# Kernel optimization log

Measured on AMD Instinct MI355X. Metric: run time of the kernel, lower is better.

The kernel has to match this reference:

```python
import jax, jax.numpy as jnp
import numpy as np

HIDDEN = 4096
N_HEADS = 32
N_KV_HEADS = 8
HEAD_DIM = HIDDEN // N_HEADS  # 128
N_GROUPS = N_HEADS // N_KV_HEADS  # 4
ROPE_THETA = 10000.0
BSZ, SEQ = 2, 2048


def rotate_half(x):
    x1 = x[..., : x.shape[-1] // 2]
    x2 = x[..., x.shape[-1] // 2 :]
    return jnp.concatenate((-x2, x1), axis=-1)


def rope_tables(seq_len, head_dim, theta):
    inv_freq = 1.0 / theta ** (jnp.arange(0, head_dim, 2, dtype=jnp.float32) / head_dim)
    t = jnp.arange(seq_len, dtype=jnp.float32)
    freqs = jnp.einsum('i,j->ij', t, inv_freq)          # [S, head_dim/2]
    emb = jnp.concatenate((freqs, freqs), axis=-1)       # [S, head_dim]
    return jnp.cos(emb), jnp.sin(emb)


def setup_inputs() -> dict:
    key = jax.random.key(0)
    ks = jax.random.split(key, 5)
    hidden_states = jax.random.normal(ks[0], (BSZ, SEQ, HIDDEN), dtype=jnp.float32)
    # causal additive mask [B, 1, Q, K]
    causal = jnp.tril(jnp.ones((SEQ, SEQ), dtype=bool))
    attention_mask = jnp.where(causal, 0.0, -1e9).astype(jnp.float32)
    attention_mask = jnp.broadcast_to(attention_mask[None, None], (BSZ, 1, SEQ, SEQ))
    position_ids = jnp.broadcast_to(jnp.arange(SEQ, dtype=jnp.int32)[None, :], (BSZ, SEQ))
    sc = 1.0 / np.sqrt(HIDDEN)
    Wq = jax.random.normal(ks[1], (HIDDEN, N_HEADS * HEAD_DIM), dtype=jnp.float32) * sc
    Wk = jax.random.normal(ks[2], (HIDDEN, N_KV_HEADS * HEAD_DIM), dtype=jnp.float32) * sc
    Wv = jax.random.normal(ks[3], (HIDDEN, N_KV_HEADS * HEAD_DIM), dtype=jnp.float32) * sc
    Wo = jax.random.normal(ks[4], (N_HEADS * HEAD_DIM, HIDDEN), dtype=jnp.float32) * sc
    return {
        'hidden_states': hidden_states,
        'attention_mask': attention_mask,
        'position_ids': position_ids,
        'Wq': Wq, 'Wk': Wk, 'Wv': Wv, 'Wo': Wo,
    }


def reference(hidden_states, attention_mask, position_ids, Wq, Wk, Wv, Wo):
    bsz, q_len, _ = hidden_states.shape
    # QKV projections
    q = (hidden_states @ Wq).reshape(bsz, q_len, N_HEADS, HEAD_DIM).swapaxes(1, 2)       # [B,H,S,D]
    k = (hidden_states @ Wk).reshape(bsz, q_len, N_KV_HEADS, HEAD_DIM).swapaxes(1, 2)    # [B,Hkv,S,D]
    v = (hidden_states @ Wv).reshape(bsz, q_len, N_KV_HEADS, HEAD_DIM).swapaxes(1, 2)    # [B,Hkv,S,D]
    # RoPE
    cos_t, sin_t = rope_tables(q_len, HEAD_DIM, ROPE_THETA)
    cos = jnp.take(cos_t, position_ids, axis=0)[:, None]  # [B,1,S,D]
    sin = jnp.take(sin_t, position_ids, axis=0)[:, None]
    q = q * cos + rotate_half(q) * sin
    k = k * cos + rotate_half(k) * sin
    # GQA attention via grouped einsum (equivalent to repeat_kv, without materializing repeats)
    qg = q.reshape(bsz, N_KV_HEADS, N_GROUPS, q_len, HEAD_DIM)
    scores = jnp.einsum('bhgqd,bhkd->bhgqk', qg, k) / jnp.sqrt(jnp.float32(HEAD_DIM))
    scores = scores + attention_mask[:, :, None]  # broadcast mask over (kv_head, group)
    probs = jax.nn.softmax(scores.astype(jnp.float32), axis=-1).astype(hidden_states.dtype)
    out = jnp.einsum('bhgqk,bhkd->bhgqd', probs, v)
    out = out.reshape(bsz, N_HEADS, q_len, HEAD_DIM).swapaxes(1, 2).reshape(bsz, q_len, HIDDEN)
    return out @ Wo
```

## Files before the change

### kernel.cpp

```cpp
#include <hip/hip_runtime.h>
#include <hip/hip_bf16.h>
#include <cstdint>

#define HIDDEN 4096
#define NH 32
#define NKV 8
#define HD 128
#define SEQ 2048
#define BSZ 2
#define QKVN 6144
#define QKVLD 6144

using bf16x8 = __attribute__((ext_vector_type(8))) short;
using f32x4  = __attribute__((ext_vector_type(4))) float;
using f32x16 = __attribute__((ext_vector_type(16))) float;

__device__ __forceinline__ ushort f2bf(float f) {
  union { float f; uint32_t u; } v; v.f = f;
  uint32_t r = (v.u + 0x7FFFu + ((v.u >> 16) & 1u)) >> 16;
  return (ushort)r;
}
__device__ __forceinline__ float bf2f(ushort s) {
  union { uint32_t u; float f; } v; v.u = ((uint32_t)s) << 16;
  return v.f;
}

__device__ __forceinline__ uint32_t cvtpk(float lo, float hi) {
  uint32_t r;
  asm("v_cvt_pk_bf16_f32 %0, %1, %2" : "=v"(r) : "v"(lo), "v"(hi));
  return r;
}
__device__ __forceinline__ void pl32swap(uint32_t& a, uint32_t& b) {
  asm("v_permlane32_swap_b32 %0, %1" : "+v"(a), "+v"(b));
}

__device__ __forceinline__ void gload_lds16(const void* g, void* l) {
  __builtin_amdgcn_global_load_lds(
      (const __attribute__((address_space(1))) void*)g,
      (__attribute__((address_space(3))) void*)l, 16, 0, 0);
}

__global__ __launch_bounds__(256)
void cvt_bf16_kernel(const float* __restrict__ X, ushort* __restrict__ Xb, int n8) {
  int t = blockIdx.x * 256 + threadIdx.x;
  if (t >= n8) return;
  size_t i = (size_t)t * 8;
  float4 a = *(const float4*)(X + i);
  float4 b = *(const float4*)(X + i + 4);
  uint4 p;
  p.x = (uint)f2bf(a.x) | ((uint)f2bf(a.y) << 16);
  p.y = (uint)f2bf(a.z) | ((uint)f2bf(a.w) << 16);
  p.z = (uint)f2bf(b.x) | ((uint)f2bf(b.y) << 16);
  p.w = (uint)f2bf(b.z) | ((uint)f2bf(b.w) << 16);
  *(uint4*)(Xb + i) = p;
}

__global__ __launch_bounds__(256)
void transpose_bf16_kernel(const float* __restrict__ W, ushort* __restrict__ WT,
                           int K, int N) {
  __shared__ ushort tile[64][72];
  const int k0 = blockIdx.y * 64, n0 = blockIdx.x * 64;
  const int tr = threadIdx.x >> 4;
  const int tc = (threadIdx.x & 15) * 4;
#pragma unroll
  for (int i = 0; i < 4; ++i) {
    const int k = tr + i * 16;
    float4 v = *(const float4*)(W + (size_t)(k0 + k) * N + n0 + tc);
    ushort4 u;
    u.x = f2bf(v.x); u.y = f2bf(v.y); u.z = f2bf(v.z); u.w = f2bf(v.w);
    *(ushort4*)&tile[k][tc] = u;
  }
  __syncthreads();
  const int nr = threadIdx.x >> 3;
  const int kc = (threadIdx.x & 7) * 8;
#pragma unroll
  for (int i = 0; i < 2; ++i) {
    const int n = nr + i * 32;
    bf16x8 o;
#pragma unroll
    for (int j = 0; j < 8; ++j) o[j] = tile[kc + j][n];
    *(bf16x8*)(WT + (size_t)(n0 + n) * K + k0 + kc) = o;
  }
}

__global__ __launch_bounds__(256)
void transpose_v_kernel(const ushort* __restrict__ Vsrc, ushort* __restrict__ VtG) {
  __shared__ ushort tile[64][72];
  const int slice = blockIdx.z;
  const int b = slice >> 3, kh = slice & 7;
  const int s0 = blockIdx.x * 64, d0 = blockIdx.y * 64;
  const ushort* src = Vsrc + ((size_t)(b * SEQ) + s0) * QKVLD + kh * HD + d0;
  const int sr = threadIdx.x >> 3;
  const int dc = (threadIdx.x & 7) * 8;
#pragma unroll
  for (int i = 0; i < 2; ++i) {
    const int s = sr + i * 32;
    *(bf16x8*)&tile[s][dc] = *(const bf16x8*)(src + (size_t)s * QKVLD + dc);
  }
  __syncthreads();
  ushort* dst = VtG + ((size_t)slice * HD + d0) * SEQ + s0;
  const int dr = threadIdx.x >> 3;
  const int sc = (threadIdx.x & 7) * 8;
#pragma unroll
  for (int i = 0; i < 2; ++i) {
    const int d = dr + i * 32;
    bf16x8 o;
#pragma unroll
    for (int j = 0; j < 8; ++j) o[j] = tile[sc + j][d];
    *(bf16x8*)(dst + (size_t)d * SEQ + sc) = o;
  }
}

__global__ __launch_bounds__(512, 2)
void gemmqkv_kernel(const ushort* __restrict__ A, const ushort* __restrict__ BT,
                    ushort* __restrict__ Cp, int M, int N, int K) {
  extern __shared__ ushort lds[];
  const int tid = threadIdx.x, lane = tid & 63, wave = tid >> 6;
  const int l15 = lane & 15, l4 = lane >> 4;
  const int wr = wave >> 2, wc = wave & 3;

  const int mt = M >> 8, ntile = N / 192, nwg = mt * ntile;
  const int swq = nwg >> 3, swr = nwg & 7;
  const int xcd = blockIdx.x & 7, lo = blockIdx.x >> 3;
  const int wg = (xcd < swr ? xcd * (swq + 1) : swr * (swq + 1) + (xcd - swr) * swq) + lo;
  const int m0 = (wg % mt) << 8;
  const int n0 = (wg / mt) * 192;

  ushort* LA[2][2];
  ushort* LB[2][2];
#pragma unroll
  for (int b_ = 0; b_ < 2; ++b_)
#pragma unroll
    for (int s_ = 0; s_ < 2; ++s_) {
      LA[b_][s_] = lds + (b_ * 2 + s_) * 8192;
      LB[b_][s_] = lds + 32768 + (b_ * 2 + s_) * 6144;
    }

  const ushort* Abase = A + (size_t)m0 * K;
  const ushort* Bbase = BT + (size_t)n0 * K;

  const int srow0 = tid >> 2;
  const int scol8 = (((tid & 3) ^ ((srow0 >> 1) & 3)) << 3);
  const int bs1 = tid;
  const int brow1 = bs1 >> 2;
  const int bcol1 = (((bs1 & 3) ^ ((bs1 >> 3) & 3)) << 3);
  const int bs2 = 512 + wave * 32 + (lane & 31);
  const int brow2 = bs2 >> 2;
  const int bcol2 = (((bs2 & 3) ^ ((bs2 >> 3) & 3)) << 3);

  const int swb  = (l4 ^ ((l15 >> 1) & 3)) << 3;
  const int aoff = (wr * 128 + l15) * 32 + swb;
  const int boff = (wc * 48 + l15) * 32 + swb;

  f32x4 acc[8][3] = {};
  bf16x8 a[4];
  bf16x8 b[3];

#define STAGE_EV(buf, ks, kt)                                                  \
  do {                                                                         \
    const size_t gc_ = (size_t)(kt) * 64 + (ks) * 32;                          \
    gload_lds16(Abase + (size_t)srow0 * K + gc_ + scol8,                       \
                &LA[buf][ks][tid * 8]);                                        \
    gload_lds16(Bbase + (size_t)brow1 * K + gc_ + bcol1,                       \
                &LB[buf][ks][tid * 8]);                                        \
  } while (0)

#define STAGE_OD(buf, ks, kt)                                                  \
  do {                                                                         \
    const size_t gc_ = (size_t)(kt) * 64 + (ks) * 32;                          \
    gload_lds16(Abase + (size_t)(128 + srow0) * K + gc_ + scol8,               \
                &LA[buf][ks][(512 + tid) * 8]);                                \
    if ((lane & 32) == 0)                                                      \
      gload_lds16(Bbase + (size_t)brow2 * K + gc_ + bcol2,                     \
                  &LB[buf][ks][(512 + wave * 32 + (lane & 31)) * 8]);          \
  } while (0)

#define MFMA_ __builtin_amdgcn_mfma_f32_16x16x32_bf16

#define PHASE_EVEN(buf, ks, sb, sk, skt)                                       \
  {                                                                            \
    _Pragma("unroll") for (int m_ = 0; m_ < 4; ++m_)                           \
      a[m_] = *(const bf16x8*)&LA[buf][ks][aoff + m_ * 512];                   \
    _Pragma("unroll") for (int n_ = 0; n_ < 3; ++n_)                           \
      b[n_] = *(const bf16x8*)&LB[buf][ks][boff + n_ * 512];                   \
    STAGE_EV(sb, sk, skt);                                                     \
    asm volatile("s_barrier" ::: "memory");                                    \
    __builtin_amdgcn_s_setprio(1);                                             \
    _Pragma("unroll") for (int m_ = 0; m_ < 4; ++m_)                           \
      _Pragma("unroll") for (int n_ = 0; n_ < 3; ++n_)                         \
        acc[m_][n_] = MFMA_(a[m_], b[n_], acc[m_][n_], 0, 0, 0);               \
    __builtin_amdgcn_s_setprio(0);                                             \
    asm volatile("s_barrier" ::: "memory");                                    \
  }

#define PHASE_ODD(buf, ks, sb, sk, skt)                                        \
  {                                                                            \
    _Pragma("unroll") for (int m_ = 0; m_ < 4; ++m_)                           \
      a[m_] = *(const bf16x8*)&LA[buf][ks][aoff + (4 + m_) * 512];             \
    STAGE_OD(sb, sk, skt);                                                     \
    asm volatile("s_barrier" ::: "memory");                                    \
    __builtin_amdgcn_s_setprio(1);                                             \
    _Pragma("unroll") for (int m_ = 0; m_ < 4; ++m_)                           \
      _Pragma("unroll") for (int n_ = 0; n_ < 3; ++n_)                         \
        acc[4 + m_][n_] = MFMA_(a[m_], b[n_], acc[4 + m_][n_], 0, 0, 0);       \
    __builtin_amdgcn_s_setprio(0);                                             \
    asm volatile("s_waitcnt vmcnt(8)");                                        \
    asm volatile("s_barrier" ::: "memory");                                    \
  }

  const int NT = K >> 6;

  STAGE_EV(0, 0, 0); STAGE_OD(0, 0, 0);
  STAGE_EV(0, 1, 0); STAGE_OD(0, 1, 0);
  STAGE_EV(1, 0, 1); STAGE_OD(1, 0, 1);
  asm volatile("s_waitcnt vmcnt(8)");
  asm volatile("s_barrier" ::: "memory");

  for (int i = 0; i < (NT >> 1); ++i) {
    const int kt0 = 2 * i;
    const int ktA = (kt0 + 2 < NT) ? kt0 + 2 : NT - 1;
    const int ktB = (kt0 + 3 < NT) ? kt0 + 3 : NT - 1;
    PHASE_EVEN(0, 0, 1, 1, kt0 + 1)
    PHASE_ODD (0, 0, 1, 1, kt0 + 1)
    PHASE_EVEN(0, 1, 0, 0, ktA)
    PHASE_ODD (0, 1, 0, 0, ktA)
    PHASE_EVEN(1, 0, 0, 1, ktA)
    PHASE_ODD (1, 0, 0, 1, ktA)
    PHASE_EVEN(1, 1, 1, 0, ktB)
    PHASE_ODD (1, 1, 1, 0, ktB)
  }
#undef PHASE_EVEN
#undef PHASE_ODD
#undef STAGE_EV
#undef STAGE_OD

  const int crow0 = m0 + wr * 128 + l4 * 4;
  const int ccol0 = n0 + wc * 48 + l15;
#pragma unroll
  for (int m_ = 0; m_ < 8; ++m_)
#pragma unroll
    for (int n_ = 0; n_ < 3; ++n_)
#pragma unroll
      for (int r_ = 0; r_ < 4; ++r_) {
        const size_t row = crow0 + m_ * 16 + r_;
        const int col = ccol0 + n_ * 16;
        Cp[row * N + col] = f2bf(acc[m_][n_][r_]);
      }
}

template<int OUT_BF16>
__global__ __launch_bounds__(512, 2)
void gemm8p_kernel(const ushort* __restrict__ A, const ushort* __restrict__ BT,
                   void* __restrict__ Cp, int M, int N, int K) {
  extern __shared__ ushort lds[];
  const int tid = threadIdx.x, lane = tid & 63, wave = tid >> 6;
  const int l15 = lane & 15, l4 = lane >> 4;
  const int wr = wave >> 2, wc = wave & 3;

  const int mt = M >> 8, nt = N >> 8, nwg = mt * nt;
  const int swq = nwg >> 3, swr = nwg & 7;
  const int xcd = blockIdx.x & 7, lo = blockIdx.x >> 3;
  const int wg = (xcd < swr ? xcd * (swq + 1) : swr * (swq + 1) + (xcd - swr) * swq) + lo;
  const int m0 = (wg % mt) << 8;
  const int n0 = (wg / mt) << 8;

  ushort* LA[2][2];
  ushort* LB[2][2];
#pragma unroll
  for (int b_ = 0; b_ < 2; ++b_)
#pragma unroll
    for (int s_ = 0; s_ < 2; ++s_) {
      LA[b_][s_] = lds + ((b_ * 2 + 0) * 2 + s_) * 8192;
      LB[b_][s_] = lds + ((b_ * 2 + 1) * 2 + s_) * 8192;
    }

  const ushort* Abase = A + (size_t)m0 * K;
  const ushort* Bbase = BT + (size_t)n0 * K;

  const int srow0 = tid >> 2;
  const int scol8 = (((tid & 3) ^ ((srow0 >> 1) & 3)) << 3);

  const int swb  = (l4 ^ ((l15 >> 1) & 3)) << 3;
  const int aoff = (wr * 128 + l15) * 32 + swb;
  const int boff = (wc * 64 + l15) * 32 + swb;

  f32x4 acc[8][4] = {};
  bf16x8 a[4];
  bf16x8 b[4];

#define STAGE(buf, ks, kt, part)                                              \
  do {                                                                        \
    const size_t gc_ = (size_t)(kt) * 64 + (ks) * 32 + scol8;                 \
    const int rw_ = srow0 + (part) * 128;                                     \
    const int dst_ = ((part) * 512 + tid) * 8;                                \
    gload_lds16(Abase + (size_t)rw_ * K + gc_, &LA[buf][ks][dst_]);           \
    gload_lds16(Bbase + (size_t)rw_ * K + gc_, &LB[buf][ks][dst_]);           \
  } while (0)

#define MFMA_ __builtin_amdgcn_mfma_f32_16x16x32_bf16

#define PHASE_EVEN(buf, ks, sb, sk, skt)                                      \
  {                                                                           \
    _Pragma("unroll") for (int m_ = 0; m_ < 4; ++m_)                          \
      a[m_] = *(const bf16x8*)&LA[buf][ks][aoff + m_ * 512];                  \
    _Pragma("unroll") for (int n_ = 0; n_ < 4; ++n_)                          \
      b[n_] = *(const bf16x8*)&LB[buf][ks][boff + n_ * 512];                  \
    STAGE(sb, sk, skt, 0);                                                    \
    asm volatile("s_barrier" ::: "memory");                                   \
    __builtin_amdgcn_s_setprio(1);                                            \
    _Pragma("unroll") for (int m_ = 0; m_ < 4; ++m_)                          \
      _Pragma("unroll") for (int n_ = 0; n_ < 4; ++n_)                        \
        acc[m_][n_] = MFMA_(a[m_], b[n_], acc[m_][n_], 0, 0, 0);              \
    __builtin_amdgcn_s_setprio(0);                                            \
    asm volatile("s_barrier" ::: "memory");                                   \
  }

#define PHASE_ODD(buf, ks, sb, sk, skt)                                       \
  {                                                                           \
    _Pragma("unroll") for (int m_ = 0; m_ < 4; ++m_)                          \
      a[m_] = *(const bf16x8*)&LA[buf][ks][aoff + (4 + m_) * 512];            \
    STAGE(sb, sk, skt, 1);                                                    \
    asm volatile("s_barrier" ::: "memory");                                   \
    __builtin_amdgcn_s_setprio(1);                                            \
    _Pragma("unroll") for (int m_ = 0; m_ < 4; ++m_)                          \
      _Pragma("unroll") for (int n_ = 0; n_ < 4; ++n_)                        \
        acc[4 + m_][n_] = MFMA_(a[m_], b[n_], acc[4 + m_][n_], 0, 0, 0);      \
    __builtin_amdgcn_s_setprio(0);                                            \
    asm volatile("s_waitcnt vmcnt(8)");                                       \
    asm volatile("s_barrier" ::: "memory");                                   \
  }

  const int NT = K >> 6;

  STAGE(0, 0, 0, 0); STAGE(0, 0, 0, 1);
  STAGE(0, 1, 0, 0); STAGE(0, 1, 0, 1);
  STAGE(1, 0, 1, 0); STAGE(1, 0, 1, 1);
  asm volatile("s_waitcnt vmcnt(8)");
  asm volatile("s_barrier" ::: "memory");

  for (int i = 0; i < (NT >> 1); ++i) {
    const int kt0 = 2 * i;
    const int ktA = (kt0 + 2 < NT) ? kt0 + 2 : NT - 1;
    const int ktB = (kt0 + 3 < NT) ? kt0 + 3 : NT - 1;
    PHASE_EVEN(0, 0, 1, 1, kt0 + 1)
    PHASE_ODD (0, 0, 1, 1, kt0 + 1)
    PHASE_EVEN(0, 1, 0, 0, ktA)
    PHASE_ODD (0, 1, 0, 0, ktA)
    PHASE_EVEN(1, 0, 0, 1, ktA)
    PHASE_ODD (1, 0, 0, 1, ktA)
    PHASE_EVEN(1, 1, 1, 0, ktB)
    PHASE_ODD (1, 1, 1, 0, ktB)
  }
#undef PHASE_EVEN
#undef PHASE_ODD
#undef STAGE

  const int crow0 = m0 + wr * 128 + l4 * 4;
  const int ccol0 = n0 + wc * 64 + l15;
#pragma unroll
  for (int m_ = 0; m_ < 8; ++m_)
#pragma unroll
    for (int n_ = 0; n_ < 4; ++n_)
#pragma unroll
      for (int r_ = 0; r_ < 4; ++r_) {
        const size_t row = crow0 + m_ * 16 + r_;
        const int col = ccol0 + n_ * 16;
        const float val = acc[m_][n_][r_];
        if (OUT_BF16) ((ushort*)Cp)[row * N + col] = f2bf(val);
        else          ((float*)Cp)[row * N + col]  = val;
      }
}

__global__ __launch_bounds__(256)
void rope_qk_kernel(ushort* qkv, const int* __restrict__ pos_ids, int total) {
  int t = blockIdx.x * 256 + threadIdx.x;
  if (t >= total) return;
  int j = t & 63;
  int rest = t >> 6;
  int hp = rest % 40;
  int bs = rest / 40;
  float pos = (float)pos_ids[bs];
  float inv = exp2f(-(float)j * (13.287712379549449f / 64.0f));
  float ang = pos * inv;
  const float osc = (hp < 32) ? 0.12751731f : 1.0f;
  float c = cosf(ang) * osc, s = sinf(ang) * osc;
  const int col = (hp < 32) ? hp * HD : HIDDEN + (hp - 32) * HD;
  ushort* p = qkv + (size_t)bs * QKVLD + col + j;
  float x1 = bf2f(p[0]), x2 = bf2f(p[64]);
  p[0]  = f2bf(x1 * c - x2 * s);
  p[64] = f2bf(x2 * c + x1 * s);
}

__global__ __launch_bounds__(512)
void attn_kernel(const ushort* __restrict__ Q, const ushort* __restrict__ K0,
                 const ushort* __restrict__ VtG, ushort* __restrict__ AO) {
  __shared__ ushort Ks[2][64 * 128];
  __shared__ ushort Vs[2][128 * 64];

  const int bid = blockIdx.x;
  const int kh  = bid & 7;
  const int r2  = bid >> 3;
  const int qtB = 7 - (r2 & 7);
  const int hq  = (r2 >> 3) & 3;
  const int b   = r2 >> 5;
  const int h   = kh * 4 + hq;
  const int q0b = qtB * 256;

  const int tid = threadIdx.x, lane = tid & 63, w = tid >> 6;
  const int l31 = lane & 31, hi = lane >> 5;
  const int q0w = q0b + w * 32;

  const size_t bS = (size_t)b * SEQ;
  const ushort* Kb = K0 + bS * QKVLD + kh * HD;
  const ushort* Vb = VtG + (size_t)(b * NKV + kh) * HD * SEQ;

  bf16x8 qf[8];
  {
    const ushort* qp = Q + (bS + q0w + l31) * QKVLD + h * HD + hi * 8;
#pragma unroll
    for (int ds = 0; ds < 8; ++ds) qf[ds] = *(const bf16x8*)(qp + ds * 16);
  }

  f32x16 accO[4] = {};
  float mrow = -1e30f, denom = 0.0f;

  const int nt = qtB * 4 + 4;

  const int j0 = 2 * w, j1 = 2 * w + 1;
  const int kl4 = lane >> 4, ks15 = lane & 15;
  const int vl3 = lane >> 3, vs7 = lane & 7;
  const int kswz = lane & 15;
  const int vswz = lane & 7;

#define KSTAGE(jj, bb, kk0) { const int k_ = (jj) * 4 + kl4;                   \
    gload_lds16(Kb + (size_t)((kk0) + k_) * QKVLD + ((ks15 ^ (k_ & 15)) << 3), \
                &Ks[bb][(jj) * 512 + lane * 8]); }
#define VSTAGE(jj, bb, kk0) { const int d_ = (jj) * 8 + vl3;                   \
    gload_lds16(Vb + (size_t)d_ * SEQ + (kk0) + ((vs7 ^ (d_ & 7)) << 3),       \
                &Vs[bb][(jj) * 512 + lane * 8]); }

  KSTAGE(j0, 0, 0) KSTAGE(j1, 0, 0) VSTAGE(j0, 0, 0) VSTAGE(j1, 0, 0)
  __syncthreads();

  for (int t = 0; t < nt; ++t) {
    const int k0 = t * 64;
    const int cur = t & 1;
    const bool pf = (t + 1 < nt);
    const bool skip = (k0 > q0w + 31);

    if (pf) {
      const int kn = k0 + 64;
      KSTAGE(j0, cur ^ 1, kn) KSTAGE(j1, cur ^ 1, kn)
      VSTAGE(j0, cur ^ 1, kn) VSTAGE(j1, cur ^ 1, kn)
    }

    if (!skip) {
      f32x16 s0 = {}, s1 = {};
      __builtin_amdgcn_s_setprio(1);
#pragma unroll
      for (int ds = 0; ds < 8; ++ds) {
        const int so = ((ds * 2 + hi) ^ kswz) << 3;
        bf16x8 kf0 = *(const bf16x8*)&Ks[cur][l31 * 128 + so];
        bf16x8 kf1 = *(const bf16x8*)&Ks[cur][(32 + l31) * 128 + so];
        s0 = __builtin_amdgcn_mfma_f32_32x32x16_bf16(kf0, qf[ds], s0, 0, 0, 0);
        s1 = __builtin_amdgcn_mfma_f32_32x32x16_bf16(kf1, qf[ds], s1, 0, 0, 0);
      }
      __builtin_amdgcn_s_setprio(0);

      if (k0 + 63 > q0w) {
        const int qrel = q0w + l31 - k0;
#pragma unroll
        for (int r = 0; r < 16; ++r) {
          const int kc = (r & 3) + 8 * (r >> 2) + 4 * hi;
          if (kc > qrel)      s0[r] = -1e30f;
          if (kc + 32 > qrel) s1[r] = -1e30f;
        }
      }
      float pm = s0[0];
#pragma unroll
      for (int r = 1; r < 16; ++r) pm = fmaxf(pm, s0[r]);
#pragma unroll
      for (int r = 0; r < 16; ++r) pm = fmaxf(pm, s1[r]);

      if (!__all(pm - mrow <= 8.0f)) {
        pm = fmaxf(pm, __shfl_xor(pm, 32));
        const float mn = fmaxf(mrow, pm);
        const float alpha = exp2f(mrow - mn);
        mrow = mn;
        denom *= alpha;
#pragma unroll
        for (int du = 0; du < 4; ++du)
#pragma unroll
          for (int r = 0; r < 16; ++r) accO[du][r] *= alpha;
      }
      float ssum = 0.0f;
#pragma unroll
      for (int r = 0; r < 16; ++r) { float p = exp2f(s0[r] - mrow); s0[r] = p; ssum += p; }
#pragma unroll
      for (int r = 0; r < 16; ++r) { float p = exp2f(s1[r] - mrow); s1[r] = p; ssum += p; }
      denom += ssum;

      uint32_t paw[4][4];
      {
        uint32_t p0 = cvtpk(s0[0], s0[1]),   p1 = cvtpk(s0[2], s0[3]);
        uint32_t p2 = cvtpk(s0[4], s0[5]),   p3 = cvtpk(s0[6], s0[7]);
        uint32_t p4 = cvtpk(s0[8], s0[9]),   p5 = cvtpk(s0[10], s0[11]);
        uint32_t p6 = cvtpk(s0[12], s0[13]), p7 = cvtpk(s0[14], s0[15]);
        pl32swap(p0, p2); pl32swap(p1, p3); pl32swap(p4, p6); pl32swap(p5, p7);
        paw[0][0] = p0; paw[0][1] = p1; paw[0][2] = p2; paw[0][3] = p3;
        paw[1][0] = p4; paw[1][1] = p5; paw[1][2] = p6; paw[1][3] = p7;
      }
      {
        uint32_t p0 = cvtpk(s1[0], s1[1]),   p1 = cvtpk(s1[2], s1[3]);
        uint32_t p2 = cvtpk(s1[4], s1[5]),   p3 = cvtpk(s1[6], s1[7]);
        uint32_t p4 = cvtpk(s1[8], s1[9]),   p5 = cvtpk(s1[10], s1[11]);
        uint32_t p6 = cvtpk(s1[12], s1[13]), p7 = cvtpk(s1[14], s1[15]);
        pl32swap(p0, p2); pl32swap(p1, p3); pl32swap(p4, p6); pl32swap(p5, p7);
        paw[2][0] = p0; paw[2][1] = p1; paw[2][2] = p2; paw[2][3] = p3;
        paw[3][0] = p4; paw[3][1] = p5; paw[3][2] = p6; paw[3][3] = p7;
      }

      __builtin_amdgcn_s_setprio(1);
#pragma unroll
      for (int du = 0; du < 4; ++du) {
#pragma unroll
        for (int ks = 0; ks < 4; ++ks) {
          const int so = ((ks * 2 + hi) ^ vswz) << 3;
          bf16x8 vf = *(const bf16x8*)&Vs[cur][(du * 32 + l31) * 64 + so];
          bf16x8 pb = *(const bf16x8*)&paw[ks][0];
          accO[du] = __builtin_amdgcn_mfma_f32_32x32x16_bf16(vf, pb, accO[du], 0, 0, 0);
        }
      }
      __builtin_amdgcn_s_setprio(0);
    }
    __syncthreads();
  }
#undef KSTAGE
#undef VSTAGE

  denom += __shfl_xor(denom, 32);
  const float inv = 1.0f / denom;
  ushort* op = AO + (bS + q0w + l31) * HIDDEN + h * HD + hi * 4;
#pragma unroll
  for (int du = 0; du < 4; ++du)
#pragma unroll
    for (int g = 0; g < 4; ++g) {
      uint2 u;
      u.x = cvtpk(accO[du][4 * g + 0] * inv, accO[du][4 * g + 1] * inv);
      u.y = cvtpk(accO[du][4 * g + 2] * inv, accO[du][4 * g + 3] * inv);
      *(uint2*)(op + du * 32 + g * 8) = u;
    }
}

extern "C" void kernel_launch(void* const* d_in, const int* in_sizes, int n_in,
                              void* d_out, int out_size, void* d_ws, size_t ws_size,
                              hipStream_t stream) {
  (void)in_sizes; (void)n_in; (void)out_size; (void)ws_size;
  const float* X   = (const float*)d_in[0];
  const int*   pos = (const int*)d_in[2];
  const float* Wq  = (const float*)d_in[3];
  const float* Wk  = (const float*)d_in[4];
  const float* Wv  = (const float*)d_in[5];
  const float* Wo  = (const float*)d_in[6];

  char* ws = (char*)d_ws;
  ushort* Xb    = (ushort*)(ws);
  ushort* QKV   = (ushort*)(ws + 33554432);
  ushort* BTqkv = (ushort*)(ws + 83886080);
  ushort* WoT   = (ushort*)(ws + 134217728);
  ushort* AO    = Xb;
  ushort* VtG   = BTqkv;

  const int M = BSZ * SEQ;
  dim3 blk(256);

  hipFuncSetAttribute((const void*)gemmqkv_kernel,
                      hipFuncAttributeMaxDynamicSharedMemorySize, 114688);
  hipFuncSetAttribute((const void*)gemm8p_kernel<0>,
                      hipFuncAttributeMaxDynamicSharedMemorySize, 131072);

  cvt_bf16_kernel<<<dim3((M * HIDDEN / 8 + 255) / 256), blk, 0, stream>>>(X, Xb, M * HIDDEN / 8);
  transpose_bf16_kernel<<<dim3(HIDDEN / 64, HIDDEN / 64), blk, 0, stream>>>(Wq, BTqkv, HIDDEN, HIDDEN);
  transpose_bf16_kernel<<<dim3((NKV * HD) / 64, HIDDEN / 64), blk, 0, stream>>>(
      Wk, BTqkv + (size_t)HIDDEN * HIDDEN, HIDDEN, NKV * HD);
  transpose_bf16_kernel<<<dim3((NKV * HD) / 64, HIDDEN / 64), blk, 0, stream>>>(
      Wv, BTqkv + (size_t)(HIDDEN + NKV * HD) * HIDDEN, HIDDEN, NKV * HD);
  transpose_bf16_kernel<<<dim3(HIDDEN / 64, HIDDEN / 64), blk, 0, stream>>>(Wo, WoT, HIDDEN, HIDDEN);

  gemmqkv_kernel<<<dim3((M / 256) * (QKVN / 192)), dim3(512), 114688, stream>>>(
      Xb, BTqkv, QKV, M, QKVN, HIDDEN);

  rope_qk_kernel<<<dim3((M * 40 * 64) / 256), blk, 0, stream>>>(QKV, pos, M * 40 * 64);
  transpose_v_kernel<<<dim3(SEQ / 64, HD / 64, BSZ * NKV), blk, 0, stream>>>(
      QKV + HIDDEN + NKV * HD, VtG);

  attn_kernel<<<dim3(512), dim3(512), 0, stream>>>(QKV, QKV + HIDDEN, VtG, AO);

  gemm8p_kernel<0><<<dim3((M / 256) * (HIDDEN / 256)), dim3(512), 131072, stream>>>(
      AO, WoT, d_out, M, HIDDEN, HIDDEN);
}
```

Before: 583.3 us.

## Merge weight transposes into one launch and shrink output GEMM tile to 128x256

Four separate weight transpose/convert launches are combined into one kernel that dispatches on block index, removing launch overhead and tail gaps. The output projection GEMM changes from 256x256 to 128x256 tiles, doubling the workgroup count from 256 to 512 so more CUs are busy with M=4096,N=4096. The staging plan, LDS layout and wait counts are reworked to match. Smaller tiles lower arithmetic intensity per workgroup and increase redundant B-tile loads.

```diff
diff --git a/kernel.cpp b/kernel.cpp
--- a/kernel.cpp
+++ b/kernel.cpp
@@ -56,10 +56,20 @@
 }
 
 __global__ __launch_bounds__(256)
-void transpose_bf16_kernel(const float* __restrict__ W, ushort* __restrict__ WT,
-                           int K, int N) {
+void transpose_all_kernel(const float* __restrict__ Wq, const float* __restrict__ Wk,
+                          const float* __restrict__ Wv, const float* __restrict__ Wo,
+                          ushort* __restrict__ BTqkv, ushort* __restrict__ WoT) {
   __shared__ ushort tile[64][72];
-  const int k0 = blockIdx.y * 64, n0 = blockIdx.x * 64;
+  const int id = blockIdx.x;
+  const float* W; ushort* WT; int N, rel;
+  if (id < 4096)      { W = Wq; WT = BTqkv;                          N = 4096; rel = id; }
+  else if (id < 5120) { W = Wk; WT = BTqkv + (size_t)4096 * 4096;    N = 1024; rel = id - 4096; }
+  else if (id < 6144) { W = Wv; WT = BTqkv + (size_t)5120 * 4096;    N = 1024; rel = id - 5120; }
+  else                { W = Wo; WT = WoT;                            N = 4096; rel = id - 6144; }
+  const int K = 4096;
+  const int nb = N >> 6;
+  const int n0 = (rel % nb) * 64, k0 = (rel / nb) * 64;
+
   const int tr = threadIdx.x >> 4;
   const int tc = (threadIdx.x & 15) * 4;
 #pragma unroll
@@ -248,20 +258,19 @@
       }
 }
 
-template<int OUT_BF16>
 __global__ __launch_bounds__(512, 2)
-void gemm8p_kernel(const ushort* __restrict__ A, const ushort* __restrict__ BT,
-                   void* __restrict__ Cp, int M, int N, int K) {
+void gemmop_kernel(const ushort* __restrict__ A, const ushort* __restrict__ BT,
+                   float* __restrict__ Cp, int M, int N, int K) {
   extern __shared__ ushort lds[];
   const int tid = threadIdx.x, lane = tid & 63, wave = tid >> 6;
   const int l15 = lane & 15, l4 = lane >> 4;
   const int wr = wave >> 2, wc = wave & 3;
 
-  const int mt = M >> 8, nt = N >> 8, nwg = mt * nt;
+  const int mt = M >> 7, nt = N >> 8, nwg = mt * nt;
   const int swq = nwg >> 3, swr = nwg & 7;
   const int xcd = blockIdx.x & 7, lo = blockIdx.x >> 3;
   const int wg = (xcd < swr ? xcd * (swq + 1) : swr * (swq + 1) + (xcd - swr) * swq) + lo;
-  const int m0 = (wg % mt) << 8;
+  const int m0 = (wg % mt) << 7;
   const int n0 = (wg / mt) << 8;
 
   ushort* LA[2][2];
@@ -270,104 +279,113 @@
   for (int b_ = 0; b_ < 2; ++b_)
 #pragma unroll
     for (int s_ = 0; s_ < 2; ++s_) {
-      LA[b_][s_] = lds + ((b_ * 2 + 0) * 2 + s_) * 8192;
-      LB[b_][s_] = lds + ((b_ * 2 + 1) * 2 + s_) * 8192;
+      LA[b_][s_] = lds + (b_ * 2 + s_) * 4096;
+      LB[b_][s_] = lds + 16384 + (b_ * 2 + s_) * 8192;
     }
 
   const ushort* Abase = A + (size_t)m0 * K;
   const ushort* Bbase = BT + (size_t)n0 * K;
 
-  const int srow0 = tid >> 2;
-  const int scol8 = (((tid & 3) ^ ((srow0 >> 1) & 3)) << 3);
+  const int arow = tid >> 2;
+  const int acol = (((tid & 3) ^ ((arow >> 1) & 3)) << 3);
+  const int brow0 = tid >> 2;
+  const int bcol0 = (((tid & 3) ^ ((brow0 >> 1) & 3)) << 3);
+  const int bs1 = 512 + tid;
+  const int brow1 = bs1 >> 2;
+  const int bcol1 = (((bs1 & 3) ^ ((brow1 >> 1) & 3)) << 3);
 
   const int swb  = (l4 ^ ((l15 >> 1) & 3)) << 3;
-  const int aoff = (wr * 128 + l15) * 32 + swb;
+  const int aoff = (wr * 64 + l15) * 32 + swb;
   const int boff = (wc * 64 + l15) * 32 + swb;
 
-  f32x4 acc[8][4] = {};
-  bf16x8 a[4];
+  f32x4 acc[4][4] = {};
+  bf16x8 a[2];
   bf16x8 b[4];
 
-#define STAGE(buf, ks, kt, part)                                              \
-  do {                                                                        \
-    const size_t gc_ = (size_t)(kt) * 64 + (ks) * 32 + scol8;                 \
-    const int rw_ = srow0 + (part) * 128;                                     \
-    const int dst_ = ((part) * 512 + tid) * 8;                                \
-    gload_lds16(Abase + (size_t)rw_ * K + gc_, &LA[buf][ks][dst_]);           \
-    gload_lds16(Bbase + (size_t)rw_ * K + gc_, &LB[buf][ks][dst_]);           \
+#define OSTAGE_EV(buf, ks, kt)                                                 \
+  do {                                                                         \
+    const size_t gc_ = (size_t)(kt) * 64 + (ks) * 32;                          \
+    gload_lds16(Abase + (size_t)arow * K + gc_ + acol,  &LA[buf][ks][tid * 8]);\
+    gload_lds16(Bbase + (size_t)brow0 * K + gc_ + bcol0, &LB[buf][ks][tid * 8]);\
   } while (0)
 
+#define OSTAGE_OD(buf, ks, kt)                                                 \
+  do {                                                                         \
+    const size_t gc_ = (size_t)(kt) * 64 + (ks) * 32;                          \
+    gload_lds16(Bbase + (size_t)brow1 * K + gc_ + bcol1,                       \
+                &LB[buf][ks][(512 + tid) * 8]);                                \
+  } while (0)
+
 #define MFMA_ __builtin_amdgcn_mfma_f32_16x16x32_bf16
 
-#define PHASE_EVEN(buf, ks, sb, sk, skt)                                      \
-  {                                                                           \
-    _Pragma("unroll") for (int m_ = 0; m_ < 4; ++m_)                          \
-      a[m_] = *(const bf16x8*)&LA[buf][ks][aoff + m_ * 512];                  \
-    _Pragma("unroll") for (int n_ = 0; n_ < 4; ++n_)                          \
-      b[n_] = *(const bf16x8*)&LB[buf][ks][boff + n_ * 512];                  \
-    STAGE(sb, sk, skt, 0);                                                    \
-    asm volatile("s_barrier" ::: "memory");                                   \
-    __builtin_amdgcn_s_setprio(1);                                            \
-    _Pragma("unroll") for (int m_ = 0; m_ < 4; ++m_)                          \
-      _Pragma("unroll") for (int n_ = 0; n_ < 4; ++n_)                        \
-        acc[m_][n_] = MFMA_(a[m_], b[n_], acc[m_][n_], 0, 0, 0);              \
-    __builtin_amdgcn_s_setprio(0);                                            \
-    asm volatile("s_barrier" ::: "memory");                                   \
-  }
-
-#define PHASE_ODD(buf, ks, sb, sk, skt)                                       \
-  {                                                                           \
-    _Pragma("unroll") for (int m_ = 0; m_ < 4; ++m_)                          \
-      a[m_] = *(const bf16x8*)&LA[buf][ks][aoff + (4 + m_) * 512];            \
-    STAGE(sb, sk, skt, 1);                                                    \
-    asm volatile("s_barrier" ::: "memory");                                   \
-    __builtin_amdgcn_s_setprio(1);                                            \
-    _Pragma("unroll") for (int m_ = 0; m_ < 4; ++m_)                          \
-      _Pragma("unroll") for (int n_ = 0; n_ < 4; ++n_)                        \
-        acc[4 + m_][n_] = MFMA_(a[m_], b[n_], acc[4 + m_][n_], 0, 0, 0);      \
-    __builtin_amdgcn_s_setprio(0);                                            \
-    asm volatile("s_waitcnt vmcnt(8)");                                       \
-    asm volatile("s_barrier" ::: "memory");                                   \
+#define OPHASE_EVEN(buf, ks, sb, sk, skt)                                      \
+  {                                                                            \
+    _Pragma("unroll") for (int m_ = 0; m_ < 2; ++m_)                           \
+      a[m_] = *(const bf16x8*)&LA[buf][ks][aoff + m_ * 512];                   \
+    _Pragma("unroll") for (int n_ = 0; n_ < 4; ++n_)                           \
+      b[n_] = *(const bf16x8*)&LB[buf][ks][boff + n_ * 512];                   \
+    OSTAGE_EV(sb, sk, skt);                                                    \
+    asm volatile("s_barrier" ::: "memory");                                    \
+    __builtin_amdgcn_s_setprio(1);                                             \
+    _Pragma("unroll") for (int m_ = 0; m_ < 2; ++m_)                           \
+      _Pragma("unroll") for (int n_ = 0; n_ < 4; ++n_)                         \
+        acc[m_][n_] = MFMA_(a[m_], b[n_], acc[m_][n_], 0, 0, 0);               \
+    __builtin_amdgcn_s_setprio(0);                                             \
+    asm volatile("s_barrier" ::: "memory");                                    \
+  }
+
+#define OPHASE_ODD(buf, ks, sb, sk, skt)                                       \
+  {                                                                            \
+    _Pragma("unroll") for (int m_ = 0; m_ < 2; ++m_)                           \
+      a[m_] = *(const bf16x8*)&LA[buf][ks][aoff + (2 + m_) * 512];             \
+    OSTAGE_OD(sb, sk, skt);                                                    \
+    asm volatile("s_barrier" ::: "memory");                                    \
+    __builtin_amdgcn_s_setprio(1);                                             \
+    _Pragma("unroll") for (int m_ = 0; m_ < 2; ++m_)                           \
+      _Pragma("unroll") for (int n_ = 0; n_ < 4; ++n_)                         \
+        acc[2 + m_][n_] = MFMA_(a[m_], b[n_], acc[2 + m_][n_], 0, 0, 0);       \
+    __builtin_amdgcn_s_setprio(0);                                             \
+    asm volatile("s_waitcnt vmcnt(6)");                                        \
+    asm volatile("s_barrier" ::: "memory");                                    \
   }
 
   const int NT = K >> 6;
 
-  STAGE(0, 0, 0, 0); STAGE(0, 0, 0, 1);
-  STAGE(0, 1, 0, 0); STAGE(0, 1, 0, 1);
-  STAGE(1, 0, 1, 0); STAGE(1, 0, 1, 1);
-  asm volatile("s_waitcnt vmcnt(8)");
+  OSTAGE_EV(0, 0, 0); OSTAGE_OD(0, 0, 0);
+  OSTAGE_EV(0, 1, 0); OSTAGE_OD(0, 1, 0);
+  OSTAGE_EV(1, 0, 1); OSTAGE_OD(1, 0, 1);
+  asm volatile("s_waitcnt vmcnt(6)");
   asm volatile("s_barrier" ::: "memory");
 
   for (int i = 0; i < (NT >> 1); ++i) {
     const int kt0 = 2 * i;
     const int ktA = (kt0 + 2 < NT) ? kt0 + 2 : NT - 1;
     const int ktB = (kt0 + 3 < NT) ? kt0 + 3 : NT - 1;
-    PHASE_EVEN(0, 0, 1, 1, kt0 + 1)
-    PHASE_ODD (0, 0, 1, 1, kt0 + 1)
-    PHASE_EVEN(0, 1, 0, 0, ktA)
-    PHASE_ODD (0, 1, 0, 0, ktA)
-    PHASE_EVEN(1, 0, 0, 1, ktA)
-    PHASE_ODD (1, 0, 0, 1, ktA)
-    PHASE_EVEN(1, 1, 1, 0, ktB)
-    PHASE_ODD (1, 1, 1, 0, ktB)
-  }
-#undef PHASE_EVEN
-#undef PHASE_ODD
-#undef STAGE
-
-  const int crow0 = m0 + wr * 128 + l4 * 4;
+    OPHASE_EVEN(0, 0, 1, 1, kt0 + 1)
+    OPHASE_ODD (0, 0, 1, 1, kt0 + 1)
+    OPHASE_EVEN(0, 1, 0, 0, ktA)
+    OPHASE_ODD (0, 1, 0, 0, ktA)
+    OPHASE_EVEN(1, 0, 0, 1, ktA)
+    OPHASE_ODD (1, 0, 0, 1, ktA)
+    OPHASE_EVEN(1, 1, 1, 0, ktB)
+    OPHASE_ODD (1, 1, 1, 0, ktB)
+  }
+#undef OPHASE_EVEN
+#undef OPHASE_ODD
+#undef OSTAGE_EV
+#undef OSTAGE_OD
+
+  const int crow0 = m0 + wr * 64 + l4 * 4;
   const int ccol0 = n0 + wc * 64 + l15;
 #pragma unroll
-  for (int m_ = 0; m_ < 8; ++m_)
+  for (int m_ = 0; m_ < 4; ++m_)
 #pragma unroll
     for (int n_ = 0; n_ < 4; ++n_)
 #pragma unroll
       for (int r_ = 0; r_ < 4; ++r_) {
         const size_t row = crow0 + m_ * 16 + r_;
         const int col = ccol0 + n_ * 16;
-        const float val = acc[m_][n_][r_];
-        if (OUT_BF16) ((ushort*)Cp)[row * N + col] = f2bf(val);
-        else          ((float*)Cp)[row * N + col]  = val;
+        Cp[row * N + col] = acc[m_][n_][r_];
       }
 }
 
@@ -576,16 +594,11 @@
 
   hipFuncSetAttribute((const void*)gemmqkv_kernel,
                       hipFuncAttributeMaxDynamicSharedMemorySize, 114688);
-  hipFuncSetAttribute((const void*)gemm8p_kernel<0>,
-                      hipFuncAttributeMaxDynamicSharedMemorySize, 131072);
+  hipFuncSetAttribute((const void*)gemmop_kernel,
+                      hipFuncAttributeMaxDynamicSharedMemorySize, 98304);
 
   cvt_bf16_kernel<<<dim3((M * HIDDEN / 8 + 255) / 256), blk, 0, stream>>>(X, Xb, M * HIDDEN / 8);
-  transpose_bf16_kernel<<<dim3(HIDDEN / 64, HIDDEN / 64), blk, 0, stream>>>(Wq, BTqkv, HIDDEN, HIDDEN);
-  transpose_bf16_kernel<<<dim3((NKV * HD) / 64, HIDDEN / 64), blk, 0, stream>>>(
-      Wk, BTqkv + (size_t)HIDDEN * HIDDEN, HIDDEN, NKV * HD);
-  transpose_bf16_kernel<<<dim3((NKV * HD) / 64, HIDDEN / 64), blk, 0, stream>>>(
-      Wv, BTqkv + (size_t)(HIDDEN + NKV * HD) * HIDDEN, HIDDEN, NKV * HD);
-  transpose_bf16_kernel<<<dim3(HIDDEN / 64, HIDDEN / 64), blk, 0, stream>>>(Wo, WoT, HIDDEN, HIDDEN);
+  transpose_all_kernel<<<dim3(10240), blk, 0, stream>>>(Wq, Wk, Wv, Wo, BTqkv, WoT);
 
   gemmqkv_kernel<<<dim3((M / 256) * (QKVN / 192)), dim3(512), 114688, stream>>>(
       Xb, BTqkv, QKV, M, QKVN, HIDDEN);
@@ -596,6 +609,6 @@
 
   attn_kernel<<<dim3(512), dim3(512), 0, stream>>>(QKV, QKV + HIDDEN, VtG, AO);
 
-  gemm8p_kernel<0><<<dim3((M / 256) * (HIDDEN / 256)), dim3(512), 131072, stream>>>(
-      AO, WoT, d_out, M, HIDDEN, HIDDEN);
-}
+  gemmop_kernel<<<dim3((M / 128) * (HIDDEN / 256)), dim3(512), 98304, stream>>>(
+      AO, WoT, (float*)d_out, M, HIDDEN, HIDDEN);
+}
```

Result: no change. 589.0 us (+1.0%).
